# Performance work log

Measured on AMD Instinct MI355X. Metric: run time of the kernel, lower is better.

## Reference

```python
import jax, jax.numpy as jnp
import numpy as np

D_MODEL = 1024
N_HEADS = 16
HEAD_DIM = D_MODEL // N_HEADS
ROPE_BASE = 100000.0
B, NT, LD = 2, 16, 128


def setup_inputs() -> dict:
    key = jax.random.key(0)
    ks = jax.random.split(key, 10)
    s = 1.0 / np.sqrt(D_MODEL)
    inp = {
        "x": jax.random.normal(ks[0], (B, NT, LD, D_MODEL), dtype=jnp.float32),
        "datetimes": jnp.sort(jax.random.randint(ks[1], (NT,), 0, 1000, dtype=jnp.int64)
                              if jax.config.jax_enable_x64 else
                              jax.random.randint(ks[1], (NT,), 0, 1000).astype(jnp.int32)),
        "Wq": jax.random.uniform(ks[2], (D_MODEL, D_MODEL), jnp.float32, -s, s),
        "bq": jnp.zeros((D_MODEL,), jnp.float32),
        "Wk": jax.random.uniform(ks[3], (D_MODEL, D_MODEL), jnp.float32, -s, s),
        "bk": jnp.zeros((D_MODEL,), jnp.float32),
        "Wv": jax.random.uniform(ks[4], (D_MODEL, D_MODEL), jnp.float32, -s, s),
        "bv": jnp.zeros((D_MODEL,), jnp.float32),
        "Wo": jax.random.uniform(ks[5], (D_MODEL, D_MODEL), jnp.float32, -s, s),
        "bo": jnp.zeros((D_MODEL,), jnp.float32),
    }
    return inp


def _rope_cos_sin(datetimes, Ld):
    # inv_freq: (head_dim/2,)
    inv_freq = 1.0 / (ROPE_BASE ** (jnp.arange(0, HEAD_DIM, 2, dtype=jnp.float32) / HEAD_DIM))
    t = datetimes.astype(jnp.float32)              # (nt,)
    freqs = jnp.outer(t, inv_freq)                 # (nt, hd/2)
    freqs = jnp.concatenate([freqs, freqs], -1)    # (nt, hd)
    freqs = jnp.repeat(freqs, Ld, axis=0)          # (nt*Ld, hd) -- each timestep expanded over Ld spatial tokens
    cos = jnp.cos(freqs)[None, None]               # (1,1,L,hd)
    sin = jnp.sin(freqs)[None, None]
    return cos, sin


def _rotate_half(v):
    h = v.shape[-1] // 2
    return jnp.concatenate([-v[..., h:], v[..., :h]], axis=-1)


def reference(x, datetimes, Wq, bq, Wk, bk, Wv, bv, Wo, bo):
    B_, nt, Ld, D = x.shape
    L = nt * Ld
    xf = x.reshape(B_, L, D)
    # projections (torch Linear: y = x @ W.T + b)
    q = (xf @ Wq.T + bq).reshape(B_, L, N_HEADS, HEAD_DIM).transpose(0, 2, 1, 3)
    k = (xf @ Wk.T + bk).reshape(B_, L, N_HEADS, HEAD_DIM).transpose(0, 2, 1, 3)
    v = (xf @ Wv.T + bv).reshape(B_, L, N_HEADS, HEAD_DIM).transpose(0, 2, 1, 3)
    cos, sin = _rope_cos_sin(datetimes, Ld)
    q = q * cos + _rotate_half(q) * sin
    k = k * cos + _rotate_half(k) * sin
    # SDPA, no mask, not causal
    scale = 1.0 / jnp.sqrt(jnp.asarray(HEAD_DIM, x.dtype))
    scores = jnp.einsum("bhqd,bhkd->bhqk", q, k) * scale
    attn = jax.nn.softmax(scores, axis=-1)
    out = jnp.einsum("bhqk,bhkd->bhqd", attn, v)
    out = out.transpose(0, 2, 1, 3).reshape(B_, nt, Ld, D)
    out = out @ Wo.T + bo
    return out, k, v
```

## Files before the change

### kernel.cpp

```cpp
#include <hip/hip_runtime.h>

typedef short bf8 __attribute__((ext_vector_type(8)));
typedef short s4v __attribute__((ext_vector_type(4)));
typedef float f4  __attribute__((ext_vector_type(4)));


__device__ __forceinline__ short f2b(float f) {
    unsigned u = __float_as_uint(f);
    u += 0x7FFFu + ((u >> 16) & 1u);
    return (short)(u >> 16);
}

__device__ __forceinline__ f4 mfma16(bf8 a, bf8 b, f4 c) {
    return __builtin_amdgcn_mfma_f32_16x16x32_bf16(a, b, c, 0, 0, 0);
}

__device__ __forceinline__ void gl_lds16(const short* g, short* l) {
    __builtin_amdgcn_global_load_lds(
        (const __attribute__((address_space(1))) void*)g,
        (__attribute__((address_space(3))) void*)l, 16, 0, 0);
}

__device__ __forceinline__ unsigned cvtpk(float lo, float hi) {
    unsigned r;
    asm("v_cvt_pk_bf16_f32 %0, %1, %2" : "=v"(r) : "v"(lo), "v"(hi));
    return r;
}

#define EXP2F(x) __builtin_amdgcn_exp2f(x)

__global__ __launch_bounds__(256) void conv_k(
    const float* __restrict__ x, const float* __restrict__ wq,
    const float* __restrict__ wk, const float* __restrict__ wv,
    const float* __restrict__ wo, const int* __restrict__ dt,
    short* __restrict__ xb, short* __restrict__ wqb, short* __restrict__ wkb,
    short* __restrict__ wvb, short* __restrict__ wob,
    float* __restrict__ ctab, float* __restrict__ stab) {
    if (blockIdx.x == 8192) {
        const int tid = threadIdx.x;
        const int ii = tid & 31;
        const float invf = exp2f(-(float)ii * (16.609640474436812f / 32.f));
        for (int t = tid >> 5; t < 16; t += 8) {
            const float a = (float)dt[t] * invf;
            ctab[t * 32 + ii] = cosf(a);
            stab[t * 32 + ii] = sinf(a);
        }
        return;
    }
    int idx = (blockIdx.x * 256 + threadIdx.x) * 4;
    const float* s; short* d; int off = idx;
    if (idx < 4194304)      { s = x;  d = xb; }
    else if (idx < 5242880) { s = wq; d = wqb; off = idx - 4194304; }
    else if (idx < 6291456) { s = wk; d = wkb; off = idx - 5242880; }
    else if (idx < 7340032) { s = wv; d = wvb; off = idx - 6291456; }
    else                    { s = wo; d = wob; off = idx - 7340032; }
    const float4 v = *(const float4*)&s[off];
    s4v o;
    o[0] = f2b(v.x); o[1] = f2b(v.y); o[2] = f2b(v.z); o[3] = f2b(v.w);
    *(s4v*)&d[off] = o;
}

__global__ __launch_bounds__(256) void gemm_qkv_k(
    const short* __restrict__ A, const short* __restrict__ W,
    const float* __restrict__ bq, const float* __restrict__ bk, const float* __restrict__ bv,
    float* __restrict__ out_k, float* __restrict__ out_v,
    short* __restrict__ qrot, short* __restrict__ kbb, short* __restrict__ vpk,
    const float* __restrict__ ctab, const float* __restrict__ stab) {
    __shared__ __align__(16) short As[2 * 4096];
    __shared__ __align__(16) short Bs[2 * 4096];

    const int n0f = blockIdx.x * 128;
    const int m0 = blockIdx.y * 128;
    const int tid = threadIdx.x;
    const int lane = tid & 63;
    const int w = tid >> 6;
    const int wr = w >> 1, wc = w & 1;
    const int g = lane >> 4, cc = lane & 15;

    const int c0 = w * 128 + lane;
    const int ar0 = c0 >> 2, ap0 = (c0 & 3) * 8;
    const short* Ag0 = A + (m0 + ar0) * 1024 + ap0;
    const short* Ag1 = Ag0 + 16 * 1024;
    const short* Wg0 = W + (n0f + ar0) * 1024 + ap0;
    const short* Wg1 = Wg0 + 16 * 1024;
    const int sof = w * 1024;

    f4 acc[4][4];
#pragma unroll
    for (int i = 0; i < 4; ++i)
#pragma unroll
        for (int j = 0; j < 4; ++j) acc[i][j] = (f4){0.f, 0.f, 0.f, 0.f};

    gl_lds16(Ag0, &As[sof]);
    gl_lds16(Ag1, &As[sof + 512]);
    gl_lds16(Wg0, &Bs[sof]);
    gl_lds16(Wg1, &Bs[sof + 512]);
    __syncthreads();

    for (int t = 0; t < 32; ++t) {
        if (t < 31) {
            const int nb = ((t + 1) & 1) * 4096;
            const int kk = (t + 1) * 32;
            gl_lds16(Ag0 + kk, &As[nb + sof]);
            gl_lds16(Ag1 + kk, &As[nb + sof + 512]);
            gl_lds16(Wg0 + kk, &Bs[nb + sof]);
            gl_lds16(Wg1 + kk, &Bs[nb + sof + 512]);
        }
        const int cb = (t & 1) * 4096;
        bf8 af[4], bfr[4];
#pragma unroll
        for (int fm = 0; fm < 4; ++fm)
            af[fm] = *(const bf8*)&As[cb + (64 * wr + 16 * fm + cc) * 32 + 8 * g];
#pragma unroll
        for (int fn = 0; fn < 4; ++fn)
            bfr[fn] = *(const bf8*)&Bs[cb + (64 * wc + 16 * fn + cc) * 32 + 8 * g];
        __builtin_amdgcn_s_setprio(1);
#pragma unroll
        for (int fm = 0; fm < 4; ++fm)
#pragma unroll
            for (int fn = 0; fn < 4; ++fn)
                acc[fm][fn] = mfma16(af[fm], bfr[fn], acc[fm][fn]);
        __builtin_amdgcn_s_setprio(0);
        __syncthreads();
    }

    const int third = n0f >> 10;
    const int n0 = n0f & 1023;
    const int h = (n0 + 64 * wc) >> 6;
    const float* bias = (third == 0) ? bq : ((third == 1) ? bk : bv);

#pragma unroll
    for (int fm = 0; fm < 4; ++fm) {
#pragma unroll
        for (int r = 0; r < 4; ++r) {
            const int m = m0 + 64 * wr + 16 * fm + 4 * g + r;
            const int b_ = m >> 11, l = m & 2047;
            const int bh2 = b_ * 16 + h;
            if (third == 2) {
                const int st2 = l >> 5, s = l & 31;
                const int j = 4 * (s >> 4) + (s & 3);
                const int g2 = (s >> 2) & 3;
#pragma unroll
                for (int fn = 0; fn < 4; ++fn) {
                    const int d = 16 * fn + cc;
                    const int n = n0 + 64 * wc + 16 * fn + cc;
                    const float val = acc[fm][fn][r] + bias[n];
                    out_v[(bh2 * 2048 + l) * 64 + d] = val;
                    const int vp = (((bh2 * 64 + st2) * 4 + g2) * 4 + (d >> 4)) * 128 + (d & 15) * 8 + j;
                    vpk[vp] = f2b(val);
                }
            } else {
                const int tt = l >> 7;
#pragma unroll
                for (int fn = 0; fn < 2; ++fn) {
                    const int d1 = 16 * fn + cc;
                    const int n1 = n0 + 64 * wc + d1;
                    const float v1 = acc[fm][fn][r] + bias[n1];
                    const float v2 = acc[fm][fn + 2][r] + bias[n1 + 32];
                    const float ct = ctab[tt * 32 + d1];
                    const float sn = stab[tt * 32 + d1];
                    const float r1 = v1 * ct - v2 * sn;
                    const float r2 = v2 * ct + v1 * sn;
                    const int oi = (bh2 * 2048 + l) * 64 + d1;
                    if (third == 0) {
                        qrot[oi]      = f2b(r1 * 0.18033688011f);
                        qrot[oi + 32] = f2b(r2 * 0.18033688011f);
                    } else {
                        out_k[oi] = r1; out_k[oi + 32] = r2;
                        const int kr = l & 31, tl = l >> 5;
                        const int kb_ = bh2 * 131072 + tl * 2048;
                        kbb[kb_ + (((kr * 128 + d1 * 2) ^ ((kr & 7) << 4)) >> 1)] = f2b(r1);
                        kbb[kb_ + (((kr * 128 + (d1 + 32) * 2) ^ ((kr & 7) << 4)) >> 1)] = f2b(r2);
                    }
                }
            }
        }
    }
}

__global__ __launch_bounds__(256) void gemm_o_k(
    const short* __restrict__ A, const short* __restrict__ W,
    const float* __restrict__ bias, float* __restrict__ out) {
    __shared__ __align__(16) short As[2 * 4096];
    __shared__ __align__(16) short Bs[2 * 2048];

    const int n0 = blockIdx.x * 64;
    const int m0 = blockIdx.y * 128;
    const int tid = threadIdx.x;
    const int lane = tid & 63;
    const int w = tid >> 6;
    const int wr = w >> 1, wc = w & 1;
    const int g = lane >> 4, cc = lane & 15;

    const int c0 = w * 128 + lane;
    const int ar0 = c0 >> 2, ap0 = (c0 & 3) * 8;
    const short* Ag0 = A + (m0 + ar0) * 1024 + ap0;
    const short* Ag1 = Ag0 + 16 * 1024;
    const int cb0 = w * 64 + lane;
    const short* Wg0 = W + (n0 + (cb0 >> 2)) * 1024 + (cb0 & 3) * 8;
    const int sofA = w * 1024, sofB = w * 512;

    f4 acc[4][2];
#pragma unroll
    for (int i = 0; i < 4; ++i) { acc[i][0] = (f4){0,0,0,0}; acc[i][1] = (f4){0,0,0,0}; }

    gl_lds16(Ag0, &As[sofA]);
    gl_lds16(Ag1, &As[sofA + 512]);
    gl_lds16(Wg0, &Bs[sofB]);
    __syncthreads();

    for (int t = 0; t < 32; ++t) {
        if (t < 31) {
            const int kk = (t + 1) * 32;
            const int nbA = ((t + 1) & 1) * 4096, nbB = ((t + 1) & 1) * 2048;
            gl_lds16(Ag0 + kk, &As[nbA + sofA]);
            gl_lds16(Ag1 + kk, &As[nbA + sofA + 512]);
            gl_lds16(Wg0 + kk, &Bs[nbB + sofB]);
        }
        const int ca = (t & 1) * 4096, cbs = (t & 1) * 2048;
        bf8 af[4], bfr[2];
#pragma unroll
        for (int fm = 0; fm < 4; ++fm)
            af[fm] = *(const bf8*)&As[ca + (64 * wr + 16 * fm + cc) * 32 + 8 * g];
#pragma unroll
        for (int fn = 0; fn < 2; ++fn)
            bfr[fn] = *(const bf8*)&Bs[cbs + (32 * wc + 16 * fn + cc) * 32 + 8 * g];
        __builtin_amdgcn_s_setprio(1);
#pragma unroll
        for (int fm = 0; fm < 4; ++fm)
#pragma unroll
            for (int fn = 0; fn < 2; ++fn)
                acc[fm][fn] = mfma16(af[fm], bfr[fn], acc[fm][fn]);
        __builtin_amdgcn_s_setprio(0);
        __syncthreads();
    }
#pragma unroll
    for (int fm = 0; fm < 4; ++fm)
#pragma unroll
        for (int r = 0; r < 4; ++r) {
            const int m = m0 + 64 * wr + 16 * fm + 4 * g + r;
#pragma unroll
            for (int fn = 0; fn < 2; ++fn) {
                const int n = n0 + 32 * wc + 16 * fn + cc;
                out[m * 1024 + n] = acc[fm][fn][r] + bias[n];
            }
        }
}

__global__ __launch_bounds__(512) void attn_k(
    const short* __restrict__ q_rot, const short* __restrict__ k_b,
    const short* __restrict__ v_pk, short* __restrict__ atb) {
    __shared__ __align__(16) short lds[24576];

    const int i = blockIdx.x;
    const int xcd = i & 7, slot = i >> 3;
    const int bh = xcd + 8 * (slot & 3);
    const int qc = slot >> 2;
    const int tid = threadIdx.x;
    const int lane = tid & 63;
    const int w = tid >> 6;
    const int g = lane >> 4, cc = lane & 15;
    const int b_ = bh >> 4, h = bh & 15;
    const int q0w = qc * 256 + w * 32;

    const short* qp = q_rot + (bh * 2048 + q0w) * 64;
    const bf8 qf00 = *(const bf8*)&qp[cc * 64 + 8 * g];
    const bf8 qf01 = *(const bf8*)&qp[cc * 64 + 32 + 8 * g];
    const bf8 qf10 = *(const bf8*)&qp[(16 + cc) * 64 + 8 * g];
    const bf8 qf11 = *(const bf8*)&qp[(16 + cc) * 64 + 32 + 8 * g];

    const int part = w >> 2, sub = w & 3;
    const short* gsrc = (part ? v_pk : k_b) + bh * 131072 + sub * 1024 + lane * 8;
    short* lbase = lds + part * 4096 + sub * 1024;

    const int swz = (cc & 7) << 4;
    const int koA0 = (cc * 128 + g * 16) ^ swz;
    const int koA1 = (cc * 128 + 64 + g * 16) ^ swz;
    const int koB0 = ((16 + cc) * 128 + g * 16) ^ swz;
    const int koB1 = ((16 + cc) * 128 + 64 + g * 16) ^ swz;
    const int vo = 8192 + g * 1024 + cc * 16;

    f4 O0[4], O1[4], Os0, Os1;
#pragma unroll
    for (int nb = 0; nb < 4; ++nb) { O0[nb] = (f4){0,0,0,0}; O1[nb] = (f4){0,0,0,0}; }
    Os0 = (f4){0, 0, 0, 0}; Os1 = (f4){0, 0, 0, 0};

    bf8 ONES;
#pragma unroll
    for (int j = 0; j < 8; ++j) ONES[j] = (short)0x3F80;

    gl_lds16(gsrc, lbase);
    gl_lds16(gsrc + 512, lbase + 512);
    gl_lds16(gsrc + 4096, lbase + 8192);
    gl_lds16(gsrc + 4096 + 512, lbase + 8192 + 512);
    asm volatile("s_waitcnt vmcnt(2)" ::: "memory");
    __builtin_amdgcn_s_barrier();

    int bufi = 0;
    for (int t = 0; t < 32; ++t) {
        if (t < 30) {
            int stg = bufi + 2; if (stg >= 3) stg -= 3;
            const short* gs = gsrc + (t + 2) * 4096;
            short* ld = lbase + stg * 8192;
            gl_lds16(gs, ld);
            gl_lds16(gs + 512, ld + 512);
        }
        const char* buf = (const char*)(lds + bufi * 8192);

#define ATTN_CHUNK(KOFF, VOFF)                                                  \
        {                                                                       \
            const bf8 ka0 = *(const bf8*)(buf + (KOFF) + koA0);                 \
            const bf8 ka1 = *(const bf8*)(buf + (KOFF) + koA1);                 \
            const bf8 kb0 = *(const bf8*)(buf + (KOFF) + koB0);                 \
            const bf8 kb1 = *(const bf8*)(buf + (KOFF) + koB1);                 \
            __builtin_amdgcn_s_setprio(1);                                      \
            f4 sA0 = (f4){0,0,0,0}, sB0 = (f4){0,0,0,0};                        \
            f4 sA1 = (f4){0,0,0,0}, sB1 = (f4){0,0,0,0};                        \
            sA0 = mfma16(ka0, qf00, sA0); sA0 = mfma16(ka1, qf01, sA0);         \
            sB0 = mfma16(kb0, qf00, sB0); sB0 = mfma16(kb1, qf01, sB0);         \
            sA1 = mfma16(ka0, qf10, sA1); sA1 = mfma16(ka1, qf11, sA1);         \
            sB1 = mfma16(kb0, qf10, sB1); sB1 = mfma16(kb1, qf11, sB1);         \
            __builtin_amdgcn_s_setprio(0);                                      \
            union { bf8 v; unsigned u[4]; } P0, P1;                             \
            P0.u[0] = cvtpk(EXP2F(sA0[0]), EXP2F(sA0[1]));                      \
            P0.u[1] = cvtpk(EXP2F(sA0[2]), EXP2F(sA0[3]));                      \
            P0.u[2] = cvtpk(EXP2F(sB0[0]), EXP2F(sB0[1]));                      \
            P0.u[3] = cvtpk(EXP2F(sB0[2]), EXP2F(sB0[3]));                      \
            P1.u[0] = cvtpk(EXP2F(sA1[0]), EXP2F(sA1[1]));                      \
            P1.u[1] = cvtpk(EXP2F(sA1[2]), EXP2F(sA1[3]));                      \
            P1.u[2] = cvtpk(EXP2F(sB1[0]), EXP2F(sB1[1]));                      \
            P1.u[3] = cvtpk(EXP2F(sB1[2]), EXP2F(sB1[3]));                      \
            const bf8 vv0 = *(const bf8*)(buf + (VOFF) + vo);                   \
            const bf8 vv1 = *(const bf8*)(buf + (VOFF) + vo + 256);             \
            const bf8 vv2 = *(const bf8*)(buf + (VOFF) + vo + 512);             \
            const bf8 vv3 = *(const bf8*)(buf + (VOFF) + vo + 768);             \
            __builtin_amdgcn_s_setprio(1);                                      \
            O0[0] = mfma16(P0.v, vv0, O0[0]); O0[1] = mfma16(P0.v, vv1, O0[1]); \
            O0[2] = mfma16(P0.v, vv2, O0[2]); O0[3] = mfma16(P0.v, vv3, O0[3]); \
            Os0 = mfma16(P0.v, ONES, Os0);                                      \
            O1[0] = mfma16(P1.v, vv0, O1[0]); O1[1] = mfma16(P1.v, vv1, O1[1]); \
            O1[2] = mfma16(P1.v, vv2, O1[2]); O1[3] = mfma16(P1.v, vv3, O1[3]); \
            Os1 = mfma16(P1.v, ONES, Os1);                                      \
            __builtin_amdgcn_s_setprio(0);                                      \
        }

        ATTN_CHUNK(0, 0)
        ATTN_CHUNK(4096, 4096)
#undef ATTN_CHUNK

        if (t < 30) { asm volatile("s_waitcnt vmcnt(2)" ::: "memory"); }
        else        { asm volatile("s_waitcnt vmcnt(0)" ::: "memory"); }
        __builtin_amdgcn_s_barrier();
        bufi = (bufi == 2) ? 0 : bufi + 1;
    }

    short* ob = atb + (b_ * 2048 + q0w) * 1024 + h * 64 + cc;
#pragma unroll
    for (int r = 0; r < 4; ++r) {
        const float i0 = 1.f / Os0[r];
        const float i1 = 1.f / Os1[r];
#pragma unroll
        for (int nb = 0; nb < 4; ++nb) {
            ob[(4 * g + r) * 1024 + nb * 16]      = f2b(O0[nb][r] * i0);
            ob[(16 + 4 * g + r) * 1024 + nb * 16] = f2b(O1[nb][r] * i1);
        }
    }
}

extern "C" void kernel_launch(void* const* d_in, const int* in_sizes, int n_in,
                              void* d_out, int out_size, void* d_ws, size_t ws_size,
                              hipStream_t stream) {
    const float* x  = (const float*)d_in[0];
    const int*   dt = (const int*)d_in[1];
    const float* Wq = (const float*)d_in[2];
    const float* bq = (const float*)d_in[3];
    const float* Wk = (const float*)d_in[4];
    const float* bk = (const float*)d_in[5];
    const float* Wv = (const float*)d_in[6];
    const float* bv = (const float*)d_in[7];
    const float* Wo = (const float*)d_in[8];
    const float* bo = (const float*)d_in[9];

    float* out   = (float*)d_out;
    float* out_k = out + 4194304;
    float* out_v = out + 8388608;

    short* xb   = (short*)d_ws;
    short* wqb  = xb + 4194304;
    short* wkb  = wqb + 1048576;
    short* wvb  = wkb + 1048576;
    short* wob  = wvb + 1048576;
    short* qrot = wob + 1048576;
    short* kbb  = qrot + 4194304;
    short* vpk  = kbb + 4194304;
    short* atb  = vpk + 4194304;
    float* ctab = (float*)(atb + 4194304);
    float* stab = ctab + 512;

    conv_k<<<8193, 256, 0, stream>>>(x, Wq, Wk, Wv, Wo, dt,
                                     xb, wqb, wkb, wvb, wob, ctab, stab);
    gemm_qkv_k<<<dim3(24, 32), 256, 0, stream>>>(xb, wqb, bq, bk, bv,
                                                 out_k, out_v, qrot, kbb, vpk, ctab, stab);
    attn_k<<<256, 512, 0, stream>>>(qrot, kbb, vpk, atb);
    gemm_o_k<<<dim3(16, 32), 256, 0, stream>>>(atb, wob, bo, out);
}
```

Baseline: 198.4 us.

## Triple-buffer GEMM LDS staging with XOR-swizzled layout and explicit vmcnt waits

Both the QKV and output projection GEMMs move from double to triple buffering in LDS, prefetching two k-tiles ahead. Partial s_waitcnt vmcnt plus raw barriers replace the full __syncthreads, so loads stay in flight across iterations. Global-to-LDS loads also XOR-swizzle the 8-element column group by row, and the fragment reads apply the same swizzle to reduce LDS bank conflicts. The cost is more LDS per block, which may lower occupancy, and correctness now depends on the hand-tuned wait counts.

```diff
diff --git a/kernel.cpp b/kernel.cpp
--- a/kernel.cpp
+++ b/kernel.cpp
@@ -66,8 +66,8 @@
     float* __restrict__ out_k, float* __restrict__ out_v,
     short* __restrict__ qrot, short* __restrict__ kbb, short* __restrict__ vpk,
     const float* __restrict__ ctab, const float* __restrict__ stab) {
-    __shared__ __align__(16) short As[2 * 4096];
-    __shared__ __align__(16) short Bs[2 * 4096];
+    __shared__ __align__(16) short As[12288];
+    __shared__ __align__(16) short Bs[12288];
 
     const int n0f = blockIdx.x * 128;
     const int m0 = blockIdx.y * 128;
@@ -77,13 +77,22 @@
     const int wr = w >> 1, wc = w & 1;
     const int g = lane >> 4, cc = lane & 15;
 
-    const int c0 = w * 128 + lane;
-    const int ar0 = c0 >> 2, ap0 = (c0 & 3) * 8;
-    const short* Ag0 = A + (m0 + ar0) * 1024 + ap0;
-    const short* Ag1 = Ag0 + 16 * 1024;
-    const short* Wg0 = W + (n0f + ar0) * 1024 + ap0;
-    const short* Wg1 = Wg0 + 16 * 1024;
-    const int sof = w * 1024;
+    const int q_ = lane & 3;
+    const int rowA0 = w * 32 + (lane >> 2);
+    const int rowA1 = rowA0 + 16;
+    const int gS = q_ ^ ((rowA0 >> 1) & 3);
+    const short* AgS0 = A + (m0 + rowA0) * 1024 + gS * 8;
+    const short* AgS1 = A + (m0 + rowA1) * 1024 + gS * 8;
+    const short* WgS0 = W + (n0f + rowA0) * 1024 + gS * 8;
+    const short* WgS1 = W + (n0f + rowA1) * 1024 + gS * 8;
+    short* dA0 = &As[w * 1024];
+    short* dA1 = &As[w * 1024 + 512];
+    short* dB0 = &Bs[w * 1024];
+    short* dB1 = &Bs[w * 1024 + 512];
+
+    const int qx = (cc >> 1) & 3;
+    const int aOfs = (64 * wr + cc) * 32 + ((g ^ qx) * 8);
+    const int bOfs = (64 * wc + cc) * 32 + ((g ^ qx) * 8);
 
     f4 acc[4][4];
 #pragma unroll
@@ -91,29 +100,32 @@
 #pragma unroll
         for (int j = 0; j < 4; ++j) acc[i][j] = (f4){0.f, 0.f, 0.f, 0.f};
 
-    gl_lds16(Ag0, &As[sof]);
-    gl_lds16(Ag1, &As[sof + 512]);
-    gl_lds16(Wg0, &Bs[sof]);
-    gl_lds16(Wg1, &Bs[sof + 512]);
-    __syncthreads();
-
+#define STAGE_QKV(T, BUF) {                                \
+        const int kk = (T) * 32;                           \
+        gl_lds16(AgS0 + kk, dA0 + (BUF) * 4096);           \
+        gl_lds16(AgS1 + kk, dA1 + (BUF) * 4096);           \
+        gl_lds16(WgS0 + kk, dB0 + (BUF) * 4096);           \
+        gl_lds16(WgS1 + kk, dB1 + (BUF) * 4096); }
+
+    STAGE_QKV(0, 0)
+    STAGE_QKV(1, 1)
+    asm volatile("s_waitcnt vmcnt(4)" ::: "memory");
+    __builtin_amdgcn_s_barrier();
+
+    int bufi = 0;
     for (int t = 0; t < 32; ++t) {
-        if (t < 31) {
-            const int nb = ((t + 1) & 1) * 4096;
-            const int kk = (t + 1) * 32;
-            gl_lds16(Ag0 + kk, &As[nb + sof]);
-            gl_lds16(Ag1 + kk, &As[nb + sof + 512]);
-            gl_lds16(Wg0 + kk, &Bs[nb + sof]);
-            gl_lds16(Wg1 + kk, &Bs[nb + sof + 512]);
-        }
-        const int cb = (t & 1) * 4096;
+        if (t < 30) {
+            int stg = bufi + 2; if (stg >= 3) stg -= 3;
+            STAGE_QKV(t + 2, stg)
+        }
+        const int cb = bufi * 4096;
         bf8 af[4], bfr[4];
 #pragma unroll
         for (int fm = 0; fm < 4; ++fm)
-            af[fm] = *(const bf8*)&As[cb + (64 * wr + 16 * fm + cc) * 32 + 8 * g];
+            af[fm] = *(const bf8*)&As[cb + aOfs + fm * 512];
 #pragma unroll
         for (int fn = 0; fn < 4; ++fn)
-            bfr[fn] = *(const bf8*)&Bs[cb + (64 * wc + 16 * fn + cc) * 32 + 8 * g];
+            bfr[fn] = *(const bf8*)&Bs[cb + bOfs + fn * 512];
         __builtin_amdgcn_s_setprio(1);
 #pragma unroll
         for (int fm = 0; fm < 4; ++fm)
@@ -121,8 +133,12 @@
             for (int fn = 0; fn < 4; ++fn)
                 acc[fm][fn] = mfma16(af[fm], bfr[fn], acc[fm][fn]);
         __builtin_amdgcn_s_setprio(0);
-        __syncthreads();
-    }
+        if (t < 30) { asm volatile("s_waitcnt vmcnt(4)" ::: "memory"); }
+        else        { asm volatile("s_waitcnt vmcnt(0)" ::: "memory"); }
+        __builtin_amdgcn_s_barrier();
+        bufi = (bufi == 2) ? 0 : bufi + 1;
+    }
+#undef STAGE_QKV
 
     const int third = n0f >> 10;
     const int n0 = n0f & 1023;
@@ -181,8 +197,8 @@
 __global__ __launch_bounds__(256) void gemm_o_k(
     const short* __restrict__ A, const short* __restrict__ W,
     const float* __restrict__ bias, float* __restrict__ out) {
-    __shared__ __align__(16) short As[2 * 4096];
-    __shared__ __align__(16) short Bs[2 * 2048];
+    __shared__ __align__(16) short As[12288];
+    __shared__ __align__(16) short Bs[6144];
 
     const int n0 = blockIdx.x * 64;
     const int m0 = blockIdx.y * 128;
@@ -192,39 +208,52 @@
     const int wr = w >> 1, wc = w & 1;
     const int g = lane >> 4, cc = lane & 15;
 
-    const int c0 = w * 128 + lane;
-    const int ar0 = c0 >> 2, ap0 = (c0 & 3) * 8;
-    const short* Ag0 = A + (m0 + ar0) * 1024 + ap0;
-    const short* Ag1 = Ag0 + 16 * 1024;
-    const int cb0 = w * 64 + lane;
-    const short* Wg0 = W + (n0 + (cb0 >> 2)) * 1024 + (cb0 & 3) * 8;
-    const int sofA = w * 1024, sofB = w * 512;
+    const int q_ = lane & 3;
+    const int rowA0 = w * 32 + (lane >> 2);
+    const int rowA1 = rowA0 + 16;
+    const int gSA = q_ ^ ((rowA0 >> 1) & 3);
+    const short* AgS0 = A + (m0 + rowA0) * 1024 + gSA * 8;
+    const short* AgS1 = A + (m0 + rowA1) * 1024 + gSA * 8;
+    const int rowB = w * 16 + (lane >> 2);
+    const int gSB = q_ ^ ((rowB >> 1) & 3);
+    const short* WgS = W + (n0 + rowB) * 1024 + gSB * 8;
+    short* dA0 = &As[w * 1024];
+    short* dA1 = &As[w * 1024 + 512];
+    short* dB  = &Bs[w * 512];
+
+    const int qx = (cc >> 1) & 3;
+    const int aOfs = (64 * wr + cc) * 32 + ((g ^ qx) * 8);
+    const int bOfs = (32 * wc + cc) * 32 + ((g ^ qx) * 8);
 
     f4 acc[4][2];
 #pragma unroll
     for (int i = 0; i < 4; ++i) { acc[i][0] = (f4){0,0,0,0}; acc[i][1] = (f4){0,0,0,0}; }
 
-    gl_lds16(Ag0, &As[sofA]);
-    gl_lds16(Ag1, &As[sofA + 512]);
-    gl_lds16(Wg0, &Bs[sofB]);
-    __syncthreads();
-
+#define STAGE_O(T, BUF) {                                  \
+        const int kk = (T) * 32;                           \
+        gl_lds16(AgS0 + kk, dA0 + (BUF) * 4096);           \
+        gl_lds16(AgS1 + kk, dA1 + (BUF) * 4096);           \
+        gl_lds16(WgS  + kk, dB  + (BUF) * 2048); }
+
+    STAGE_O(0, 0)
+    STAGE_O(1, 1)
+    asm volatile("s_waitcnt vmcnt(3)" ::: "memory");
+    __builtin_amdgcn_s_barrier();
+
+    int bufi = 0;
     for (int t = 0; t < 32; ++t) {
-        if (t < 31) {
-            const int kk = (t + 1) * 32;
-            const int nbA = ((t + 1) & 1) * 4096, nbB = ((t + 1) & 1) * 2048;
-            gl_lds16(Ag0 + kk, &As[nbA + sofA]);
-            gl_lds16(Ag1 + kk, &As[nbA + sofA + 512]);
-            gl_lds16(Wg0 + kk, &Bs[nbB + sofB]);
-        }
-        const int ca = (t & 1) * 4096, cbs = (t & 1) * 2048;
+        if (t < 30) {
+            int stg = bufi + 2; if (stg >= 3) stg -= 3;
+            STAGE_O(t + 2, stg)
+        }
+        const int cbA = bufi * 4096, cbB = bufi * 2048;
         bf8 af[4], bfr[2];
 #pragma unroll
         for (int fm = 0; fm < 4; ++fm)
-            af[fm] = *(const bf8*)&As[ca + (64 * wr + 16 * fm + cc) * 32 + 8 * g];
+            af[fm] = *(const bf8*)&As[cbA + aOfs + fm * 512];
 #pragma unroll
         for (int fn = 0; fn < 2; ++fn)
-            bfr[fn] = *(const bf8*)&Bs[cbs + (32 * wc + 16 * fn + cc) * 32 + 8 * g];
+            bfr[fn] = *(const bf8*)&Bs[cbB + bOfs + fn * 512];
         __builtin_amdgcn_s_setprio(1);
 #pragma unroll
         for (int fm = 0; fm < 4; ++fm)
@@ -232,8 +261,13 @@
             for (int fn = 0; fn < 2; ++fn)
                 acc[fm][fn] = mfma16(af[fm], bfr[fn], acc[fm][fn]);
         __builtin_amdgcn_s_setprio(0);
-        __syncthreads();
-    }
+        if (t < 30) { asm volatile("s_waitcnt vmcnt(3)" ::: "memory"); }
+        else        { asm volatile("s_waitcnt vmcnt(0)" ::: "memory"); }
+        __builtin_amdgcn_s_barrier();
+        bufi = (bufi == 2) ? 0 : bufi + 1;
+    }
+#undef STAGE_O
+
 #pragma unroll
     for (int fm = 0; fm < 4; ++fm)
 #pragma unroll
```

After: 198.5 us. About the same (+0.0%).
